# Performance work log

Hardware: AMD Instinct MI355X
Metric: run time of the kernel (lower is better)

## Reference

```python
import jax, jax.numpy as jnp
import numpy as np

N = 100000   # nodes
E = 1600000  # edges (avg degree 16)
D = 64       # in_dim == hidden_dim
L = 3        # num_layers
EPS = 1e-5   # LayerNorm eps


def setup_inputs() -> dict:
    key = jax.random.key(0)
    k0, k1, k2 = jax.random.split(key, 3)
    x = jax.random.normal(k0, (N, D), dtype=jnp.float32)
    edge_index = jax.random.randint(k1, (2, E), 0, N, dtype=jnp.int32)
    # Per-layer GCN weights/bias (Glorot-ish scale) and LayerNorm params
    Ws = jax.random.normal(k2, (L, D, D), dtype=jnp.float32) / np.float32(np.sqrt(D))
    bs = jnp.zeros((L, D), dtype=jnp.float32)
    gammas = jnp.ones((L, D), dtype=jnp.float32)
    betas = jnp.zeros((L, D), dtype=jnp.float32)
    return {"x": x, "Ws": Ws, "bs": bs, "gammas": gammas, "betas": betas,
            "edge_index": edge_index}


def _layer_norm(h, gamma, beta):
    mu = jnp.mean(h, axis=-1, keepdims=True)
    var = jnp.mean(jnp.square(h - mu), axis=-1, keepdims=True)
    return (h - mu) * jax.lax.rsqrt(var + EPS) * gamma + beta


def reference(x, Ws, bs, gammas, betas, edge_index):
    # GCNConv semantics: add self-loops, symmetric deg^{-1/2} normalization.
    loop = jnp.arange(N, dtype=edge_index.dtype)
    row = jnp.concatenate([edge_index[0], loop])  # source (gather)
    col = jnp.concatenate([edge_index[1], loop])  # target (scatter)
    deg = jax.ops.segment_sum(jnp.ones_like(col, dtype=x.dtype), col, num_segments=N)
    dinv = jnp.where(deg > 0, jax.lax.rsqrt(deg), jnp.zeros_like(deg))
    enorm = dinv[row] * dinv[col]  # (E+N,)

    h = x
    for i in range(L):
        hw = h @ Ws[i]                                   # (N, D) small GEMM
        msg = hw[row] * enorm[:, None]                   # (E+N, D) gather
        h = jax.ops.segment_sum(msg, col, num_segments=N) + bs[i]  # scatter-add
        h = _layer_norm(h, gammas[i], betas[i])
        if i < L - 1:
            h = jax.nn.relu(h)                           # dropout is identity in eval
    return h
```

## Files before the change

### kernel.cpp

```cpp
#include <hip/hip_runtime.h>
#include <hip/hip_bf16.h>


#define DDIM 64
#define EPSV 1e-5f
#define BSHIFT 8
#define BNODES (1 << BSHIFT)
#define NBUCK 512
#define CAP 5120
#define CHUNK 4096

typedef __hip_bfloat16 bf16;
typedef unsigned int u32;
typedef unsigned short u16;
typedef unsigned long long u64;
typedef __attribute__((ext_vector_type(8))) short frag8;
typedef __attribute__((ext_vector_type(4))) float f32x4;

__device__ __forceinline__ float b2f(bf16 v) { return __bfloat162float(v); }
__device__ __forceinline__ float lo2f(u32 u) {
    union { u32 x; float f; } c; c.x = u << 16; return c.f;
}
__device__ __forceinline__ float hi2f(u32 u) {
    union { u32 x; float f; } c; c.x = u & 0xffff0000u; return c.f;
}
__device__ __forceinline__ u32 packbf(float a, float b) {
    union { bf16 h; u16 u; } ca, cb;
    ca.h = __float2bfloat16(a);
    cb.h = __float2bfloat16(b);
    return (u32)ca.u | ((u32)cb.u << 16);
}
__device__ __forceinline__ float cvt_load(const void* src, int i, int f32) {
    return f32 ? ((const float*)src)[i] : b2f(((const bf16*)src)[i]);
}


__global__ void __launch_bounds__(512) partition_edges(const int* __restrict__ row,
                                                       const int* __restrict__ col,
                                                       int* __restrict__ gcur,
                                                       u32* __restrict__ pairs,
                                                       const u32* __restrict__ g,
                                                       int* __restrict__ flagF32, int E) {
    __shared__ int hist[NBUCK];
    __shared__ int gbase[NBUCK];
    __shared__ int lcur[NBUCK];
    int tid = threadIdx.x;
    int chunk0 = blockIdx.x * CHUNK;
    if (blockIdx.x == 0 && tid == 0) *flagF32 = (g[0] == 0x3F800000u) ? 1 : 0;
    hist[tid] = 0;
    lcur[tid] = 0;
    __syncthreads();
    int r[CHUNK / 512], c[CHUNK / 512];
#pragma unroll
    for (int i = 0; i < CHUNK / 512; i++) {
        int idx = chunk0 + i * 512 + tid;
        if (idx < E) {
            r[i] = row[idx];
            c[i] = col[idx];
            atomicAdd(&hist[c[i] >> BSHIFT], 1);
        }
    }
    __syncthreads();
    int h = hist[tid];
    int gb = (h > 0) ? atomicAdd(&gcur[tid], h) : 0;
    if (gb + h > CAP) gb = CAP - h;
    gbase[tid] = tid * CAP + gb;
    __syncthreads();
#pragma unroll
    for (int i = 0; i < CHUNK / 512; i++) {
        int idx = chunk0 + i * 512 + tid;
        if (idx < E) {
            int b = c[i] >> BSHIFT;
            int pos = gbase[b] + atomicAdd(&lcur[b], 1);
            pairs[(size_t)pos] = ((u32)(c[i] & (BNODES - 1)) << 24) | (u32)r[i];
        }
    }
}

__global__ void __launch_bounds__(512) build_csr(const u32* __restrict__ pairs,
                                                 const int* __restrict__ gcur,
                                                 int* __restrict__ ptr,
                                                 int* __restrict__ pend,
                                                 int* __restrict__ srcs,
                                                 float* __restrict__ dinv,
                                                 const void* __restrict__ W,
                                                 const void* __restrict__ bsv,
                                                 const void* __restrict__ gsv,
                                                 const void* __restrict__ btv,
                                                 bf16* __restrict__ dWt,
                                                 bf16* __restrict__ db,
                                                 bf16* __restrict__ dg,
                                                 bf16* __restrict__ dbt,
                                                 const int* __restrict__ flagF32,
                                                 int nbuck, int N, int E) {
    __shared__ int deg[BNODES];
    __shared__ int lptr[BNODES];
    __shared__ int lfill[BNODES];
    int b = blockIdx.x;
    int tid = threadIdx.x;
    if (b >= nbuck) {
        int f = *flagF32;
        for (int i = tid; i < 3 * 4096; i += 512) {
            int L = i >> 12, n = (i >> 6) & 63, k = i & 63;
            dWt[i] = __float2bfloat16(cvt_load(W, (L << 12) | (k << 6) | n, f));
        }
        for (int i = tid; i < 192; i += 512) {
            db[i]  = __float2bfloat16(cvt_load(bsv, i, f));
            dg[i]  = __float2bfloat16(cvt_load(gsv, i, f));
            dbt[i] = __float2bfloat16(cvt_load(btv, i, f));
        }
        return;
    }
    int node0 = b << BSHIFT;
    int nn = min(BNODES, N - node0);
    if (tid < BNODES) { deg[tid] = 0; lfill[tid] = 0; }
    __syncthreads();
    int beg = b * CAP;
    int ecnt = gcur[b];
    if (ecnt > CAP) ecnt = CAP;
    int end = beg + ecnt;
    for (int i = beg + tid; i < end; i += 512)
        atomicAdd(&deg[pairs[i] >> 24], 1);
    __syncthreads();
    int d = (tid < BNODES) ? deg[tid] : 0;
    if (tid < BNODES) lptr[tid] = d;
    __syncthreads();
    for (int off = 1; off < BNODES; off <<= 1) {
        int t = (tid >= off && tid < BNODES) ? lptr[tid - off] : 0;
        __syncthreads();
        if (tid < BNODES) lptr[tid] += t;
        __syncthreads();
    }
    int excl = (tid < BNODES) ? lptr[tid] - d : 0;
    if (tid < BNODES) lptr[tid] = beg + excl;
    if (tid < nn) {
        ptr[node0 + tid]  = beg + excl;
        pend[node0 + tid] = beg + excl + d;
        dinv[node0 + tid] = rsqrtf((float)(d + 1));
    }
    __syncthreads();
    for (int i = beg + tid; i < end; i += 512) {
        u32 pr = pairs[i];
        int li = pr >> 24;
        int p = lptr[li] + atomicAdd(&lfill[li], 1);
        srcs[p] = (int)(pr & 0xFFFFFFu);
    }
}

__global__ void __launch_bounds__(256) convert_h(const void* __restrict__ x,
                                                 const float* __restrict__ dinv,
                                                 bf16* __restrict__ H,
                                                 const int* __restrict__ flagF32,
                                                 int nX8) {
    int i = blockIdx.x * 256 + threadIdx.x;
    if (i >= nX8) return;
    int f = *flagF32;
    float dv = dinv[i >> 3];
    uint4 out;
    if (f) {
        const float4* p = (const float4*)((const float*)x + (size_t)i * 8);
        float4 u = p[0], v = p[1];
        out.x = packbf(u.x * dv, u.y * dv);
        out.y = packbf(u.z * dv, u.w * dv);
        out.z = packbf(v.x * dv, v.y * dv);
        out.w = packbf(v.z * dv, v.w * dv);
    } else {
        uint4 u = *(const uint4*)((const bf16*)x + (size_t)i * 8);
        out.x = packbf(lo2f(u.x) * dv, hi2f(u.x) * dv);
        out.y = packbf(lo2f(u.y) * dv, hi2f(u.y) * dv);
        out.z = packbf(lo2f(u.z) * dv, hi2f(u.z) * dv);
        out.w = packbf(lo2f(u.w) * dv, hi2f(u.w) * dv);
    }
    ((uint4*)H)[i] = out;
}


#define LOADG(g) \
    if (m > (g) * 8) { \
        int s0 = __shfl(sidx, bl + (g) * 8 + sub, 64); \
        int s1 = __shfl(sidx, bl + (g) * 8 + 4 + sub, 64); \
        qa##g = ((const uint4*)(Hs + ((size_t)s0 << 6)))[quad]; \
        qb##g = ((const uint4*)(Hs + ((size_t)s1 << 6)))[quad]; \
    }

#define FMAG(g) \
    if (m > (g) * 8) { \
        float k0 = ((g) * 8 + sub < m) ? 1.f : 0.f; \
        float k1 = ((g) * 8 + 4 + sub < m) ? 1.f : 0.f; \
        a0 = fmaf(lo2f(qa##g.x), k0, a0); a1 = fmaf(hi2f(qa##g.x), k0, a1); \
        a2 = fmaf(lo2f(qa##g.y), k0, a2); a3 = fmaf(hi2f(qa##g.y), k0, a3); \
        a4 = fmaf(lo2f(qa##g.z), k0, a4); a5 = fmaf(hi2f(qa##g.z), k0, a5); \
        a6 = fmaf(lo2f(qa##g.w), k0, a6); a7 = fmaf(hi2f(qa##g.w), k0, a7); \
        a0 = fmaf(lo2f(qb##g.x), k1, a0); a1 = fmaf(hi2f(qb##g.x), k1, a1); \
        a2 = fmaf(lo2f(qb##g.y), k1, a2); a3 = fmaf(hi2f(qb##g.y), k1, a3); \
        a4 = fmaf(lo2f(qb##g.z), k1, a4); a5 = fmaf(hi2f(qb##g.z), k1, a5); \
        a6 = fmaf(lo2f(qb##g.w), k1, a6); a7 = fmaf(hi2f(qb##g.w), k1, a7); \
    }

__global__ void __launch_bounds__(256, 4) fused_layer(const bf16* __restrict__ Hs,
                                                      const int* __restrict__ ptr,
                                                      const int* __restrict__ pend,
                                                      const int* __restrict__ srcs,
                                                      const float* __restrict__ dinv,
                                                      const bf16* __restrict__ Wt,
                                                      const bf16* __restrict__ bias,
                                                      const bf16* __restrict__ gamma,
                                                      const bf16* __restrict__ beta,
                                                      bf16* __restrict__ outB,
                                                      float* __restrict__ outF,
                                                      const int* __restrict__ flagF32,
                                                      const float* __restrict__ dscale,
                                                      int relu, int last, int N) {
    __shared__ __align__(16) bf16 lsA[4][16][64];
    int tid = threadIdx.x;
    int wv = tid >> 6, lane = tid & 63;
    int half = lane >> 5, lane32 = lane & 31;
    int sub = lane32 >> 3, quad = lane & 7;
    int r0 = blockIdx.x * 64 + wv * 16;

    int myrow = r0 + (lane & 15);
    int mb = 0, me = 0;
    float mdv = 0.f;
    if (myrow < N) {
        mb = ptr[myrow];
        me = pend[myrow];
        mdv = dinv[myrow];
    }

    int sid0[8];
#pragma unroll
    for (int it = 0; it < 8; it++) {
        int rl = it * 2 + half;
        int pb = __shfl(mb, rl, 64);
        int dd = __shfl(me, rl, 64) - pb;
        int s = 0;
        if (lane32 < dd) s = srcs[pb + lane32];
        sid0[it] = s;
    }

#pragma unroll
    for (int it = 0; it < 8; it++) {
        int rl = it * 2 + half;
        int v = r0 + rl;
        int vc = v < N ? v : N - 1;
        uint4 selfq = ((const uint4*)(Hs + ((size_t)vc << 6)))[quad];
        int beg = __shfl(mb, rl, 64);
        int end = __shfl(me, rl, 64);
        int m = end - beg;
        if (m > 32) m = 32;
        int sidx = sid0[it];
        int bl = half << 5;
        uint4 qa0, qb0, qa1, qb1, qa2, qb2, qa3, qb3;
        LOADG(0)
        LOADG(1)
        LOADG(2)
        LOADG(3)
        float a0 = 0.f, a1 = 0.f, a2 = 0.f, a3 = 0.f;
        float a4 = 0.f, a5 = 0.f, a6 = 0.f, a7 = 0.f;
        FMAG(0)
        FMAG(1)
        FMAG(2)
        FMAG(3)
        for (int base = beg + 32; base < end; base += 32) {
            int rem = end - base;
            int m2 = rem < 32 ? rem : 32;
            int sx = 0;
            if (lane32 < m2) sx = srcs[base + lane32];
            for (int j = 0; j < m2; j += 8) {
                int e0 = j + sub;
                int e1 = j + 4 + sub;
                int s0 = __shfl(sx, bl + e0, 64);
                int s1 = __shfl(sx, bl + e1, 64);
                float k0 = (e0 < m2) ? 1.f : 0.f;
                float k1 = (e1 < m2) ? 1.f : 0.f;
                uint4 q0 = ((const uint4*)(Hs + ((size_t)s0 << 6)))[quad];
                uint4 q1 = ((const uint4*)(Hs + ((size_t)s1 << 6)))[quad];
                a0 = fmaf(lo2f(q0.x), k0, a0); a1 = fmaf(hi2f(q0.x), k0, a1);
                a2 = fmaf(lo2f(q0.y), k0, a2); a3 = fmaf(hi2f(q0.y), k0, a3);
                a4 = fmaf(lo2f(q0.z), k0, a4); a5 = fmaf(hi2f(q0.z), k0, a5);
                a6 = fmaf(lo2f(q0.w), k0, a6); a7 = fmaf(hi2f(q0.w), k0, a7);
                a0 = fmaf(lo2f(q1.x), k1, a0); a1 = fmaf(hi2f(q1.x), k1, a1);
                a2 = fmaf(lo2f(q1.y), k1, a2); a3 = fmaf(hi2f(q1.y), k1, a3);
                a4 = fmaf(lo2f(q1.z), k1, a4); a5 = fmaf(hi2f(q1.z), k1, a5);
                a6 = fmaf(lo2f(q1.w), k1, a6); a7 = fmaf(hi2f(q1.w), k1, a7);
            }
        }
#pragma unroll
        for (int d = 8; d < 32; d <<= 1) {
            a0 += __shfl_xor(a0, d, 64); a1 += __shfl_xor(a1, d, 64);
            a2 += __shfl_xor(a2, d, 64); a3 += __shfl_xor(a3, d, 64);
            a4 += __shfl_xor(a4, d, 64); a5 += __shfl_xor(a5, d, 64);
            a6 += __shfl_xor(a6, d, 64); a7 += __shfl_xor(a7, d, 64);
        }
        float dv = __shfl(mdv, rl, 64);
        if (sub == 0 && v < N) {
            a0 += lo2f(selfq.x); a1 += hi2f(selfq.x);
            a2 += lo2f(selfq.y); a3 += hi2f(selfq.y);
            a4 += lo2f(selfq.z); a5 += hi2f(selfq.z);
            a6 += lo2f(selfq.w); a7 += hi2f(selfq.w);
            uint4 o;
            o.x = packbf(a0 * dv, a1 * dv);
            o.y = packbf(a2 * dv, a3 * dv);
            o.z = packbf(a4 * dv, a5 * dv);
            o.w = packbf(a6 * dv, a7 * dv);
            *(uint4*)&lsA[wv][rl][quad * 8] = o;
        }
    }

    int n = lane & 15, q = lane >> 4;
    frag8 af0 = *(const frag8*)&lsA[wv][n][q * 8];
    frag8 af1 = *(const frag8*)&lsA[wv][n][32 + q * 8];

    f32x4 acc[4];
#pragma unroll
    for (int t = 0; t < 4; t++) acc[t] = (f32x4){0.f, 0.f, 0.f, 0.f};
#pragma unroll
    for (int t = 0; t < 4; t++) {
        const uint4* bp = (const uint4*)(Wt + (((size_t)(t * 16 + n)) << 6));
        frag8 bf0 = __builtin_bit_cast(frag8, bp[q]);
        frag8 bf1 = __builtin_bit_cast(frag8, bp[4 + q]);
        acc[t] = __builtin_amdgcn_mfma_f32_16x16x32_bf16(af0, bf0, acc[t], 0, 0, 0);
        acc[t] = __builtin_amdgcn_mfma_f32_16x16x32_bf16(af1, bf1, acc[t], 0, 0, 0);
    }

    float bb[4], gg[4], be[4];
#pragma unroll
    for (int t = 0; t < 4; t++) {
        int c = t * 16 + n;
        bb[t] = b2f(bias[c]);
        gg[t] = b2f(gamma[c]);
        be[t] = b2f(beta[c]);
    }
    int f32o = last ? flagF32[0] : 0;

#pragma unroll
    for (int r = 0; r < 4; r++) {
        int rr = r0 + q * 4 + r;
        float v0 = acc[0][r] + bb[0];
        float v1 = acc[1][r] + bb[1];
        float v2 = acc[2][r] + bb[2];
        float v3 = acc[3][r] + bb[3];
        float s = v0 + v1 + v2 + v3;
        s += __shfl_xor(s, 1, 64);
        s += __shfl_xor(s, 2, 64);
        s += __shfl_xor(s, 4, 64);
        s += __shfl_xor(s, 8, 64);
        float mu = s * (1.f / 64.f);
        float d0 = v0 - mu, d1 = v1 - mu, d2 = v2 - mu, d3 = v3 - mu;
        float sq = d0 * d0 + d1 * d1 + d2 * d2 + d3 * d3;
        sq += __shfl_xor(sq, 1, 64);
        sq += __shfl_xor(sq, 2, 64);
        sq += __shfl_xor(sq, 4, 64);
        sq += __shfl_xor(sq, 8, 64);
        float rs = rsqrtf(sq * (1.f / 64.f) + EPSV);
        float o0 = d0 * rs * gg[0] + be[0];
        float o1 = d1 * rs * gg[1] + be[1];
        float o2 = d2 * rs * gg[2] + be[2];
        float o3 = d3 * rs * gg[3] + be[3];
        if (relu) {
            o0 = fmaxf(o0, 0.f); o1 = fmaxf(o1, 0.f);
            o2 = fmaxf(o2, 0.f); o3 = fmaxf(o3, 0.f);
        }
        if (rr < N) {
            if (dscale) {
                float sc = dscale[rr];
                o0 *= sc; o1 *= sc; o2 *= sc; o3 *= sc;
            }
            size_t base = ((size_t)rr << 6) + n;
            if (f32o) {
                outF[base] = o0; outF[base + 16] = o1;
                outF[base + 32] = o2; outF[base + 48] = o3;
            } else {
                outB[base] = __float2bfloat16(o0);
                outB[base + 16] = __float2bfloat16(o1);
                outB[base + 32] = __float2bfloat16(o2);
                outB[base + 48] = __float2bfloat16(o3);
            }
        }
    }
}


extern "C" void kernel_launch(void* const* d_in, const int* in_sizes, int n_in,
                              void* d_out, int out_size, void* d_ws, size_t ws_size,
                              hipStream_t stream) {
    (void)n_in; (void)out_size; (void)ws_size;
    const void* x      = d_in[0];
    const void* Wsrc   = d_in[1];
    const void* bsrc   = d_in[2];
    const void* gsrc   = d_in[3];
    const void* btsrc  = d_in[4];
    const int*  ei     = (const int*)d_in[5];
    int N = in_sizes[0] / DDIM;
    int E = in_sizes[5] / 2;
    const int* rowp = ei;
    const int* colp = ei + E;

    int nbuck = (N + BNODES - 1) >> BSHIFT;

    char* w = (char*)d_ws;
    auto alloc = [&](size_t bytes) -> char* {
        char* p = w;
        w += (bytes + 255) / 256 * 256;
        return p;
    };
    int*   flag  = (int*)alloc(4);
    int*   gcur  = (int*)alloc(NBUCK * 4);
    int*   ptr   = (int*)alloc((size_t)N * 4);
    int*   pend  = (int*)alloc((size_t)N * 4);
    int*   srcs  = (int*)alloc((size_t)nbuck * CAP * 4);
    float* dinv  = (float*)alloc((size_t)N * 4);
    bf16*  H     = (bf16*)alloc((size_t)N * DDIM * 2);
    u32*   pairs = (u32*)alloc((size_t)nbuck * CAP * 4);
    bf16*  wsW   = (bf16*)alloc((size_t)3 * 4096 * 2);
    bf16*  wsB   = (bf16*)alloc(192 * 2);
    bf16*  wsG   = (bf16*)alloc(192 * 2);
    bf16*  wsBt  = (bf16*)alloc(192 * 2);
    bf16*  H2    = (bf16*)alloc((size_t)N * DDIM * 2);

    const int tb = 256;
    hipMemsetAsync(gcur, 0, NBUCK * 4, stream);
    partition_edges<<<(E + CHUNK - 1) / CHUNK, 512, 0, stream>>>(rowp, colp, gcur,
                                                                 pairs, (const u32*)gsrc,
                                                                 flag, E);
    build_csr<<<nbuck + 1, 512, 0, stream>>>(pairs, gcur, ptr, pend, srcs, dinv,
                                             Wsrc, bsrc, gsrc, btsrc,
                                             wsW, wsB, wsG, wsBt,
                                             flag, nbuck, N, E);

    int nX8 = N * DDIM / 8;
    convert_h<<<(nX8 + tb - 1) / tb, tb, 0, stream>>>(x, dinv, H, flag, nX8);

    int gBlocks = (N + 63) / 64;
    fused_layer<<<gBlocks, tb, 0, stream>>>(H, ptr, pend, srcs, dinv,
                                            wsW + 0 * 4096, wsB + 0,   wsG + 0,   wsBt + 0,
                                            H2, nullptr, flag, dinv, 1, 0, N);
    fused_layer<<<gBlocks, tb, 0, stream>>>(H2, ptr, pend, srcs, dinv,
                                            wsW + 1 * 4096, wsB + 64,  wsG + 64,  wsBt + 64,
                                            H, nullptr, flag, dinv, 1, 0, N);
    fused_layer<<<gBlocks, tb, 0, stream>>>(H, ptr, pend, srcs, dinv,
                                            wsW + 2 * 4096, wsB + 128, wsG + 128, wsBt + 128,
                                            (bf16*)d_out, (float*)d_out, flag, nullptr, 0, 1, N);
}
```

Measured before the change: 237.8 us.

## Replace bucketed CSR build with fixed-capacity per-node adjacency via global atomics

```diff
diff --git a/kernel.cpp b/kernel.cpp
--- a/kernel.cpp
+++ b/kernel.cpp
@@ -4,16 +4,11 @@
 
 #define DDIM 64
 #define EPSV 1e-5f
-#define BSHIFT 8
-#define BNODES (1 << BSHIFT)
-#define NBUCK 512
-#define CAP 5120
-#define CHUNK 4096
+#define NCAP 64
 
 typedef __hip_bfloat16 bf16;
 typedef unsigned int u32;
 typedef unsigned short u16;
-typedef unsigned long long u64;
 typedef __attribute__((ext_vector_type(8))) short frag8;
 typedef __attribute__((ext_vector_type(4))) float f32x4;
 
@@ -34,55 +29,35 @@
     return f32 ? ((const float*)src)[i] : b2f(((const bf16*)src)[i]);
 }
 
-
-__global__ void __launch_bounds__(512) partition_edges(const int* __restrict__ row,
-                                                       const int* __restrict__ col,
-                                                       int* __restrict__ gcur,
-                                                       u32* __restrict__ pairs,
-                                                       const u32* __restrict__ g,
-                                                       int* __restrict__ flagF32, int E) {
-    __shared__ int hist[NBUCK];
-    __shared__ int gbase[NBUCK];
-    __shared__ int lcur[NBUCK];
-    int tid = threadIdx.x;
-    int chunk0 = blockIdx.x * CHUNK;
-    if (blockIdx.x == 0 && tid == 0) *flagF32 = (g[0] == 0x3F800000u) ? 1 : 0;
-    hist[tid] = 0;
-    lcur[tid] = 0;
-    __syncthreads();
-    int r[CHUNK / 512], c[CHUNK / 512];
-#pragma unroll
-    for (int i = 0; i < CHUNK / 512; i++) {
-        int idx = chunk0 + i * 512 + tid;
-        if (idx < E) {
-            r[i] = row[idx];
-            c[i] = col[idx];
-            atomicAdd(&hist[c[i] >> BSHIFT], 1);
-        }
-    }
-    __syncthreads();
-    int h = hist[tid];
-    int gb = (h > 0) ? atomicAdd(&gcur[tid], h) : 0;
-    if (gb + h > CAP) gb = CAP - h;
-    gbase[tid] = tid * CAP + gb;
-    __syncthreads();
-#pragma unroll
-    for (int i = 0; i < CHUNK / 512; i++) {
-        int idx = chunk0 + i * 512 + tid;
-        if (idx < E) {
-            int b = c[i] >> BSHIFT;
-            int pos = gbase[b] + atomicAdd(&lcur[b], 1);
-            pairs[(size_t)pos] = ((u32)(c[i] & (BNODES - 1)) << 24) | (u32)r[i];
-        }
-    }
-}
-
-__global__ void __launch_bounds__(512) build_csr(const u32* __restrict__ pairs,
-                                                 const int* __restrict__ gcur,
-                                                 int* __restrict__ ptr,
-                                                 int* __restrict__ pend,
-                                                 int* __restrict__ srcs,
-                                                 float* __restrict__ dinv,
+__global__ void __launch_bounds__(256) partition_direct(const int* __restrict__ row,
+                                                        const int* __restrict__ col,
+                                                        int* __restrict__ ndeg,
+                                                        int* __restrict__ srcs,
+                                                        const u32* __restrict__ g,
+                                                        int* __restrict__ flagF32, int E) {
+    int gid = blockIdx.x * 256 + threadIdx.x;
+    if (gid == 0) *flagF32 = (g[0] == 0x3F800000u) ? 1 : 0;
+    int E4 = E >> 2;
+    int stride = gridDim.x * 256;
+    for (int i = gid; i < E4; i += stride) {
+        int4 r = ((const int4*)row)[i];
+        int4 c = ((const int4*)col)[i];
+        int p;
+        p = atomicAdd(&ndeg[c.x], 1); if (p < NCAP) srcs[(c.x << 6) + p] = r.x;
+        p = atomicAdd(&ndeg[c.y], 1); if (p < NCAP) srcs[(c.y << 6) + p] = r.y;
+        p = atomicAdd(&ndeg[c.z], 1); if (p < NCAP) srcs[(c.z << 6) + p] = r.z;
+        p = atomicAdd(&ndeg[c.w], 1); if (p < NCAP) srcs[(c.w << 6) + p] = r.w;
+    }
+    for (int i = (E4 << 2) + gid; i < E; i += stride) {
+        int cc = col[i];
+        int p = atomicAdd(&ndeg[cc], 1);
+        if (p < NCAP) srcs[(cc << 6) + p] = row[i];
+    }
+}
+
+__global__ void __launch_bounds__(256) convert_h(const void* __restrict__ x,
+                                                 const int* __restrict__ ndeg,
+                                                 bf16* __restrict__ H,
                                                  const void* __restrict__ W,
                                                  const void* __restrict__ bsv,
                                                  const void* __restrict__ gsv,
@@ -92,70 +67,24 @@
                                                  bf16* __restrict__ dg,
                                                  bf16* __restrict__ dbt,
                                                  const int* __restrict__ flagF32,
-                                                 int nbuck, int N, int E) {
-    __shared__ int deg[BNODES];
-    __shared__ int lptr[BNODES];
-    __shared__ int lfill[BNODES];
-    int b = blockIdx.x;
-    int tid = threadIdx.x;
-    if (b >= nbuck) {
-        int f = *flagF32;
-        for (int i = tid; i < 3 * 4096; i += 512) {
+                                                 int nX8) {
+    int f = *flagF32;
+    if (blockIdx.x == gridDim.x - 1) {
+        int tid = threadIdx.x;
+        for (int i = tid; i < 3 * 4096; i += 256) {
             int L = i >> 12, n = (i >> 6) & 63, k = i & 63;
             dWt[i] = __float2bfloat16(cvt_load(W, (L << 12) | (k << 6) | n, f));
         }
-        for (int i = tid; i < 192; i += 512) {
+        for (int i = tid; i < 192; i += 256) {
             db[i]  = __float2bfloat16(cvt_load(bsv, i, f));
             dg[i]  = __float2bfloat16(cvt_load(gsv, i, f));
             dbt[i] = __float2bfloat16(cvt_load(btv, i, f));
         }
         return;
     }
-    int node0 = b << BSHIFT;
-    int nn = min(BNODES, N - node0);
-    if (tid < BNODES) { deg[tid] = 0; lfill[tid] = 0; }
-    __syncthreads();
-    int beg = b * CAP;
-    int ecnt = gcur[b];
-    if (ecnt > CAP) ecnt = CAP;
-    int end = beg + ecnt;
-    for (int i = beg + tid; i < end; i += 512)
-        atomicAdd(&deg[pairs[i] >> 24], 1);
-    __syncthreads();
-    int d = (tid < BNODES) ? deg[tid] : 0;
-    if (tid < BNODES) lptr[tid] = d;
-    __syncthreads();
-    for (int off = 1; off < BNODES; off <<= 1) {
-        int t = (tid >= off && tid < BNODES) ? lptr[tid - off] : 0;
-        __syncthreads();
-        if (tid < BNODES) lptr[tid] += t;
-        __syncthreads();
-    }
-    int excl = (tid < BNODES) ? lptr[tid] - d : 0;
-    if (tid < BNODES) lptr[tid] = beg + excl;
-    if (tid < nn) {
-        ptr[node0 + tid]  = beg + excl;
-        pend[node0 + tid] = beg + excl + d;
-        dinv[node0 + tid] = rsqrtf((float)(d + 1));
-    }
-    __syncthreads();
-    for (int i = beg + tid; i < end; i += 512) {
-        u32 pr = pairs[i];
-        int li = pr >> 24;
-        int p = lptr[li] + atomicAdd(&lfill[li], 1);
-        srcs[p] = (int)(pr & 0xFFFFFFu);
-    }
-}
-
-__global__ void __launch_bounds__(256) convert_h(const void* __restrict__ x,
-                                                 const float* __restrict__ dinv,
-                                                 bf16* __restrict__ H,
-                                                 const int* __restrict__ flagF32,
-                                                 int nX8) {
     int i = blockIdx.x * 256 + threadIdx.x;
     if (i >= nX8) return;
-    int f = *flagF32;
-    float dv = dinv[i >> 3];
+    float dv = rsqrtf((float)(ndeg[i >> 3] + 1));
     uint4 out;
     if (f) {
         const float4* p = (const float4*)((const float*)x + (size_t)i * 8);
@@ -198,10 +127,8 @@
     }
 
 __global__ void __launch_bounds__(256, 4) fused_layer(const bf16* __restrict__ Hs,
-                                                      const int* __restrict__ ptr,
-                                                      const int* __restrict__ pend,
+                                                      const int* __restrict__ ndeg,
                                                       const int* __restrict__ srcs,
-                                                      const float* __restrict__ dinv,
                                                       const bf16* __restrict__ Wt,
                                                       const bf16* __restrict__ bias,
                                                       const bf16* __restrict__ gamma,
@@ -209,7 +136,7 @@
                                                       bf16* __restrict__ outB,
                                                       float* __restrict__ outF,
                                                       const int* __restrict__ flagF32,
-                                                      const float* __restrict__ dscale,
+                                                      int premult,
                                                       int relu, int last, int N) {
     __shared__ __align__(16) bf16 lsA[4][16][64];
     int tid = threadIdx.x;
@@ -219,13 +146,12 @@
     int r0 = blockIdx.x * 64 + wv * 16;
 
     int myrow = r0 + (lane & 15);
-    int mb = 0, me = 0;
-    float mdv = 0.f;
-    if (myrow < N) {
-        mb = ptr[myrow];
-        me = pend[myrow];
-        mdv = dinv[myrow];
-    }
+    int dg = 0;
+    if (myrow < N) dg = ndeg[myrow];
+    int dgc = dg > NCAP ? NCAP : dg;
+    int mb = myrow << 6;
+    int me = mb + dgc;
+    float mdv = rsqrtf((float)(dg + 1));
 
     int sid0[8];
 #pragma unroll
@@ -362,8 +288,8 @@
             o2 = fmaxf(o2, 0.f); o3 = fmaxf(o3, 0.f);
         }
         if (rr < N) {
-            if (dscale) {
-                float sc = dscale[rr];
+            if (premult) {
+                float sc = rsqrtf((float)(ndeg[rr] + 1));
                 o0 *= sc; o1 *= sc; o2 *= sc; o3 *= sc;
             }
             size_t base = ((size_t)rr << 6) + n;
@@ -396,8 +322,6 @@
     const int* rowp = ei;
     const int* colp = ei + E;
 
-    int nbuck = (N + BNODES - 1) >> BSHIFT;
-
     char* w = (char*)d_ws;
     auto alloc = [&](size_t bytes) -> char* {
         char* p = w;
@@ -405,13 +329,9 @@
         return p;
     };
     int*   flag  = (int*)alloc(4);
-    int*   gcur  = (int*)alloc(NBUCK * 4);
-    int*   ptr   = (int*)alloc((size_t)N * 4);
-    int*   pend  = (int*)alloc((size_t)N * 4);
-    int*   srcs  = (int*)alloc((size_t)nbuck * CAP * 4);
-    float* dinv  = (float*)alloc((size_t)N * 4);
+    int*   ndeg  = (int*)alloc((size_t)N * 4);
+    int*   srcs  = (int*)alloc((size_t)N * NCAP * 4);
     bf16*  H     = (bf16*)alloc((size_t)N * DDIM * 2);
-    u32*   pairs = (u32*)alloc((size_t)nbuck * CAP * 4);
     bf16*  wsW   = (bf16*)alloc((size_t)3 * 4096 * 2);
     bf16*  wsB   = (bf16*)alloc(192 * 2);
     bf16*  wsG   = (bf16*)alloc(192 * 2);
@@ -419,26 +339,27 @@
     bf16*  H2    = (bf16*)alloc((size_t)N * DDIM * 2);
 
     const int tb = 256;
-    hipMemsetAsync(gcur, 0, NBUCK * 4, stream);
-    partition_edges<<<(E + CHUNK - 1) / CHUNK, 512, 0, stream>>>(rowp, colp, gcur,
-                                                                 pairs, (const u32*)gsrc,
-                                                                 flag, E);
-    build_csr<<<nbuck + 1, 512, 0, stream>>>(pairs, gcur, ptr, pend, srcs, dinv,
-                                             Wsrc, bsrc, gsrc, btsrc,
-                                             wsW, wsB, wsG, wsBt,
-                                             flag, nbuck, N, E);
+    hipMemsetAsync(ndeg, 0, (size_t)N * 4, stream);
+
+    int pBlocks = (E / 4 + tb - 1) / tb;
+    partition_direct<<<pBlocks, tb, 0, stream>>>(rowp, colp, ndeg, srcs,
+                                                 (const u32*)gsrc, flag, E);
 
     int nX8 = N * DDIM / 8;
-    convert_h<<<(nX8 + tb - 1) / tb, tb, 0, stream>>>(x, dinv, H, flag, nX8);
+    int cBlocks = (nX8 + tb - 1) / tb + 1;
+    convert_h<<<cBlocks, tb, 0, stream>>>(x, ndeg, H,
+                                          Wsrc, bsrc, gsrc, btsrc,
+                                          wsW, wsB, wsG, wsBt,
+                                          flag, nX8);
 
     int gBlocks = (N + 63) / 64;
-    fused_layer<<<gBlocks, tb, 0, stream>>>(H, ptr, pend, srcs, dinv,
+    fused_layer<<<gBlocks, tb, 0, stream>>>(H, ndeg, srcs,
                                             wsW + 0 * 4096, wsB + 0,   wsG + 0,   wsBt + 0,
-                                            H2, nullptr, flag, dinv, 1, 0, N);
-    fused_layer<<<gBlocks, tb, 0, stream>>>(H2, ptr, pend, srcs, dinv,
+                                            H2, nullptr, flag, 1, 1, 0, N);
+    fused_layer<<<gBlocks, tb, 0, stream>>>(H2, ndeg, srcs,
                                             wsW + 1 * 4096, wsB + 64,  wsG + 64,  wsBt + 64,
-                                            H, nullptr, flag, dinv, 1, 0, N);
-    fused_layer<<<gBlocks, tb, 0, stream>>>(H, ptr, pend, srcs, dinv,
+                                            H, nullptr, flag, 1, 1, 0, N);
+    fused_layer<<<gBlocks, tb, 0, stream>>>(H, ndeg, srcs,
                                             wsW + 2 * 4096, wsB + 128, wsG + 128, wsBt + 128,
-                                            (bf16*)d_out, (float*)d_out, flag, nullptr, 0, 1, N);
-}
+                                            (bf16*)d_out, (float*)d_out, flag, 0, 0, 1, N);
+}
```

Measured after the change: 346.6 us. 45.7% more time.
